# Optimization experiments

Hardware: AMD Instinct MI355X
Metric: run time of the kernel (lower is better)

## Reference

```python
import jax, jax.numpy as jnp
import numpy as np

H = 1024
R = 16


def setup_inputs() -> dict:
    key = jax.random.key(0)
    ks = jax.random.split(key, 9)
    s = 1.0 / np.sqrt(H)
    x = jax.random.normal(ks[0], (8192, H), dtype=jnp.float32)
    # gate (rule_attention): Linear(H, R)
    Wa = jax.random.uniform(ks[1], (H, R), minval=-s, maxval=s, dtype=jnp.float32)
    ba = jax.random.uniform(ks[2], (R,), minval=-s, maxval=s, dtype=jnp.float32)
    # stacked rule_heads: R x (Linear(H,H) -> ReLU -> Linear(H,H))
    W1 = jax.random.uniform(ks[3], (R, H, H), minval=-s, maxval=s, dtype=jnp.float32)
    b1 = jax.random.uniform(ks[4], (R, H), minval=-s, maxval=s, dtype=jnp.float32)
    W2 = jax.random.uniform(ks[5], (R, H, H), minval=-s, maxval=s, dtype=jnp.float32)
    b2 = jax.random.uniform(ks[6], (R, H), minval=-s, maxval=s, dtype=jnp.float32)
    # stacked rule_confidence: R x (Linear(H,1) -> Sigmoid)
    Wc = jax.random.uniform(ks[7], (R, H), minval=-s, maxval=s, dtype=jnp.float32)
    bc = jax.random.uniform(ks[8], (R,), minval=-s, maxval=s, dtype=jnp.float32)
    return {"x": x, "Wa": Wa, "ba": ba, "W1": W1, "b1": b1,
            "W2": W2, "b2": b2, "Wc": Wc, "bc": bc}


def reference(x, Wa, ba, W1, b1, W2, b2, Wc, bc):
    # gate: softmax over rules               [B, R]
    attention = jax.nn.softmax(x @ Wa + ba, axis=-1)
    # all rule MLPs as one batched matmul    [B, R, H]
    h = jax.nn.relu(jnp.einsum("bh,rhd->brd", x, W1) + b1)
    outputs = jnp.einsum("brd,rdo->bro", h, W2) + b2
    # per-rule confidence                    [B, R]
    confidences = jax.nn.sigmoid(jnp.einsum("bh,rh->br", x, Wc) + bc)
    # combine gate with confidence, renormalize, weighted sum over rules
    combined = attention * confidences
    combined = combined / (combined.sum(axis=-1, keepdims=True) + 1e-8)
    output = jnp.einsum("bro,br->bo", outputs, combined)  # [B, H]
    return output, confidences
```

## Files before the change

kernel.cpp:

```cpp
#include <hip/hip_runtime.h>

typedef __attribute__((ext_vector_type(8))) short short8;
typedef __attribute__((ext_vector_type(4))) float f32x4;

#define B_SZ 8192
#define H_SZ 1024
#define R_SZ 16

__device__ __forceinline__ unsigned short f2bf(float f) {
  union { float f; unsigned u; } v; v.f = f;
  unsigned u = v.u + 0x7FFFu + ((v.u >> 16) & 1u);
  return (unsigned short)(u >> 16);
}

__global__ __launch_bounds__(256) void cvt_bf16(const float* __restrict__ s,
                                                unsigned short* __restrict__ d) {
  size_t i = ((size_t)blockIdx.x * 256 + threadIdx.x) * 8;
  float4 f0 = *(const float4*)(s + i);
  float4 f1 = *(const float4*)(s + i + 4);
  short8 v;
  v[0] = (short)f2bf(f0.x); v[1] = (short)f2bf(f0.y);
  v[2] = (short)f2bf(f0.z); v[3] = (short)f2bf(f0.w);
  v[4] = (short)f2bf(f1.x); v[5] = (short)f2bf(f1.y);
  v[6] = (short)f2bf(f1.z); v[7] = (short)f2bf(f1.w);
  *(short8*)(d + i) = v;
}

__global__ __launch_bounds__(256) void transpose_cvt(const float* __restrict__ src,
                                                     unsigned short* __restrict__ dst,
                                                     int rows, int cols) {
  __shared__ float t[32][33];
  size_t zoff = (size_t)blockIdx.z * (size_t)rows * cols;
  int c0 = blockIdx.x * 32, r0 = blockIdx.y * 32;
  int tx = threadIdx.x, ty = threadIdx.y;
#pragma unroll
  for (int i = 0; i < 4; ++i)
    t[ty + 8 * i][tx] = src[zoff + (size_t)(r0 + ty + 8 * i) * cols + c0 + tx];
  __syncthreads();
#pragma unroll
  for (int i = 0; i < 4; ++i)
    dst[zoff + (size_t)(c0 + ty + 8 * i) * rows + r0 + tx] = f2bf(t[tx][ty + 8 * i]);
}

__global__ __launch_bounds__(64) void gate_kernel(const float* __restrict__ x,
                                                  const float* __restrict__ Wa,
                                                  const float* __restrict__ ba,
                                                  const float* __restrict__ Wc,
                                                  const float* __restrict__ bc,
                                                  float* __restrict__ comb,
                                                  float* __restrict__ conf) {
  int b = blockIdx.x, l = threadIdx.x;
  const float* xr = x + (size_t)b * H_SZ;
  float xv[16];
#pragma unroll
  for (int j = 0; j < 16; ++j) xv[j] = xr[l + 64 * j];
  float la[16], lcf[16];
#pragma unroll
  for (int r = 0; r < 16; ++r) {
    float sa = 0.f, sc = 0.f;
#pragma unroll
    for (int j = 0; j < 16; ++j) {
      int h = l + 64 * j;
      sa += xv[j] * Wa[h * 16 + r];
      sc += xv[j] * Wc[r * H_SZ + h];
    }
#pragma unroll
    for (int off = 32; off > 0; off >>= 1) {
      sa += __shfl_xor(sa, off);
      sc += __shfl_xor(sc, off);
    }
    la[r] = sa + ba[r];
    lcf[r] = sc + bc[r];
  }
  float mx = la[0];
#pragma unroll
  for (int r = 1; r < 16; ++r) mx = fmaxf(mx, la[r]);
  float se = 0.f;
#pragma unroll
  for (int r = 0; r < 16; ++r) { la[r] = expf(la[r] - mx); se += la[r]; }
  float cb[16]; float cs = 0.f;
#pragma unroll
  for (int r = 0; r < 16; ++r) {
    float cf = 1.f / (1.f + expf(-lcf[r]));
    lcf[r] = cf;
    cb[r] = (la[r] / se) * cf;
    cs += cb[r];
  }
  float inv = 1.f / (cs + 1e-8f);
  if (l < 16) {
    float cv = 0.f, qv = 0.f;
#pragma unroll
    for (int r = 0; r < 16; ++r)
      if (r == l) { cv = lcf[r]; qv = cb[r] * inv; }
    conf[b * 16 + l] = cv;
    comb[b * 16 + l] = qv;
  }
}

template <int MODE>
__global__ __launch_bounds__(256) void gemm_nt(
    const unsigned short* __restrict__ A, int lda,
    const unsigned short* __restrict__ B, int ldb, int K,
    unsigned short* __restrict__ Hp, int ldh,
    const float* __restrict__ b1v,
    float* __restrict__ Out,
    const float* __restrict__ b2v,
    const float* __restrict__ comb,
    int r_base, int accum) {
  __shared__ short smem[16384];
  short* As = smem;
  short* Bs = smem + 8192;

  const int tid = threadIdx.x;
  const int lane = tid & 63;
  const int wid = tid >> 6;
  const int wm = wid >> 1, wn = wid & 1;
  const int lr = lane >> 4, lc = lane & 15;

  const int bn0 = blockIdx.x * 128;
  const int bm0 = blockIdx.y * 128;

  int srow[4], ssc[4];
#pragma unroll
  for (int i = 0; i < 4; ++i) {
    int idx = i * 256 + tid;
    srow[i] = idx >> 3;
    ssc[i] = idx & 7;
  }

  const f32x4 zero = {0.f, 0.f, 0.f, 0.f};
  f32x4 acc[4][4];
#pragma unroll
  for (int i = 0; i < 4; ++i)
#pragma unroll
    for (int j = 0; j < 4; ++j) acc[i][j] = zero;

  const int KT = K >> 6;

  short8 va[4], vb[4];
#pragma unroll
  for (int i = 0; i < 4; ++i) {
    va[i] = *(const short8*)(A + (size_t)(bm0 + srow[i]) * lda + ssc[i] * 8);
    vb[i] = *(const short8*)(B + (size_t)(bn0 + srow[i]) * ldb + ssc[i] * 8);
  }

  for (int kt = 0; kt < KT; ++kt) {
    __syncthreads();
#pragma unroll
    for (int i = 0; i < 4; ++i) {
      *(short8*)(As + srow[i] * 64 + ((ssc[i] ^ (srow[i] & 7)) * 8)) = va[i];
      *(short8*)(Bs + srow[i] * 64 + ((ssc[i] ^ (srow[i] & 7)) * 8)) = vb[i];
    }
    __syncthreads();
    if (kt + 1 < KT) {
      int k0 = (kt + 1) << 6;
#pragma unroll
      for (int i = 0; i < 4; ++i) {
        va[i] = *(const short8*)(A + (size_t)(bm0 + srow[i]) * lda + k0 + ssc[i] * 8);
        vb[i] = *(const short8*)(B + (size_t)(bn0 + srow[i]) * ldb + k0 + ssc[i] * 8);
      }
    }
#pragma unroll
    for (int c = 0; c < 2; ++c) {
      short8 af[4], bfr[4];
#pragma unroll
      for (int f = 0; f < 4; ++f) {
        int ra = wm * 64 + f * 16 + lc;
        af[f] = *(const short8*)(As + ra * 64 + (((c * 4 + lr) ^ (ra & 7)) * 8));
        int rb = wn * 64 + f * 16 + lc;
        bfr[f] = *(const short8*)(Bs + rb * 64 + (((c * 4 + lr) ^ (rb & 7)) * 8));
      }
#pragma unroll
      for (int mf = 0; mf < 4; ++mf)
#pragma unroll
        for (int nf = 0; nf < 4; ++nf)
          acc[mf][nf] = __builtin_amdgcn_mfma_f32_16x16x32_bf16(af[mf], bfr[nf],
                                                                acc[mf][nf], 0, 0, 0);
    }
  }

#pragma unroll
  for (int mf = 0; mf < 4; ++mf) {
#pragma unroll
    for (int nf = 0; nf < 4; ++nf) {
      int m0 = bm0 + wm * 64 + mf * 16 + lr * 4;
      int n = bn0 + wn * 64 + nf * 16 + lc;
      f32x4 a = acc[mf][nf];
      if (MODE == 0) {
        int r = r_base + (n >> 10);
        int d = n & 1023;
        float bias = b1v[r * H_SZ + d];
#pragma unroll
        for (int j = 0; j < 4; ++j) {
          float v = fmaxf(a[j] + bias, 0.f) * comb[(size_t)(m0 + j) * 16 + r];
          Hp[(size_t)(m0 + j) * ldh + n] = f2bf(v);
        }
      } else {
#pragma unroll
        for (int j = 0; j < 4; ++j) {
          size_t row = (size_t)(m0 + j);
          float v = a[j];
          if (accum) {
            v += Out[row * H_SZ + n];
          } else {
            float bs = 0.f;
#pragma unroll
            for (int r = 0; r < 16; ++r)
              bs += comb[row * 16 + r] * b2v[r * H_SZ + n];
            v += bs;
          }
          Out[row * H_SZ + n] = v;
        }
      }
    }
  }
}

extern "C" void kernel_launch(void* const* d_in, const int* in_sizes, int n_in,
                              void* d_out, int out_size, void* d_ws, size_t ws_size,
                              hipStream_t stream) {
  if (n_in < 9) return;
  const float* x  = (const float*)d_in[0];
  const float* Wa = (const float*)d_in[1];
  const float* ba = (const float*)d_in[2];
  const float* W1 = (const float*)d_in[3];
  const float* b1 = (const float*)d_in[4];
  const float* W2 = (const float*)d_in[5];
  const float* b2 = (const float*)d_in[6];
  const float* Wc = (const float*)d_in[7];
  const float* bc = (const float*)d_in[8];

  float* out = (float*)d_out;
  float* conf = out + (size_t)B_SZ * H_SZ;

  char* w = (char*)d_ws;
  unsigned short* xb = (unsigned short*)w;  w += (size_t)B_SZ * H_SZ * 2;
  unsigned short* W1T = (unsigned short*)w; w += (size_t)R_SZ * H_SZ * H_SZ * 2;
  unsigned short* W2T = (unsigned short*)w; w += (size_t)R_SZ * H_SZ * H_SZ * 2;
  float* comb = (float*)w;                  w += (size_t)B_SZ * R_SZ * 4;
  unsigned short* Hp = (unsigned short*)w;
  size_t used = (size_t)(w - (char*)d_ws);

  int G = 16;
  while (G > 1 && used + (size_t)B_SZ * G * H_SZ * 2 > ws_size) G >>= 1;
  if (used + (size_t)B_SZ * G * H_SZ * 2 > ws_size) return;

  cvt_bf16<<<dim3((B_SZ * H_SZ) / (256 * 8)), dim3(256), 0, stream>>>(x, xb);
  dim3 tb(32, 8);
  transpose_cvt<<<dim3(32, 32, 16), tb, 0, stream>>>(W1, W1T, H_SZ, H_SZ);
  transpose_cvt<<<dim3(32, 512, 1), tb, 0, stream>>>(W2, W2T, R_SZ * H_SZ, H_SZ);
  gate_kernel<<<dim3(B_SZ), dim3(64), 0, stream>>>(x, Wa, ba, Wc, bc, comb, conf);

  int ngroups = R_SZ / G;
  for (int g = 0; g < ngroups; ++g) {
    gemm_nt<0><<<dim3(G * 8, 64), dim3(256), 0, stream>>>(
        xb, H_SZ,
        W1T + (size_t)g * G * H_SZ * H_SZ, H_SZ, H_SZ,
        Hp, G * H_SZ, b1, nullptr, nullptr, comb, g * G, 0);
    gemm_nt<1><<<dim3(8, 64), dim3(256), 0, stream>>>(
        Hp, G * H_SZ,
        W2T + (size_t)g * G * H_SZ, R_SZ * H_SZ, G * H_SZ,
        nullptr, 0, nullptr, out, b2, comb, 0, (g > 0) ? 1 : 0);
  }
}
```

Baseline: 780.1 us.

## Double-buffer GEMM tiles via direct global-to-LDS loads and coalesce gate weights

The GEMM main loop now loads each tile straight into LDS with global_load_lds into two alternating buffers. The next K-tile's loads are issued before the MFMAs on the current tile run, replacing the register-staged prefetch and its two barriers per step. LDS use doubles to 64KB per block, which may lower occupancy. The gate kernel now reads a transposed copy of Wa so the loads coalesce, and it packs four rows per 256-thread block.

```diff
diff --git a/kernel.cpp b/kernel.cpp
--- a/kernel.cpp
+++ b/kernel.cpp
@@ -42,14 +42,22 @@
     dst[zoff + (size_t)(c0 + ty + 8 * i) * rows + r0 + tx] = f2bf(t[tx][ty + 8 * i]);
 }
 
-__global__ __launch_bounds__(64) void gate_kernel(const float* __restrict__ x,
-                                                  const float* __restrict__ Wa,
-                                                  const float* __restrict__ ba,
-                                                  const float* __restrict__ Wc,
-                                                  const float* __restrict__ bc,
-                                                  float* __restrict__ comb,
-                                                  float* __restrict__ conf) {
-  int b = blockIdx.x, l = threadIdx.x;
+__global__ __launch_bounds__(256) void transpose_wa(const float* __restrict__ Wa,
+                                                    float* __restrict__ WaT) {
+  int t = blockIdx.x * 256 + threadIdx.x;
+  int h = t >> 4, r = t & 15;
+  WaT[r * H_SZ + h] = Wa[t];
+}
+
+__global__ __launch_bounds__(256) void gate_kernel(const float* __restrict__ x,
+                                                   const float* __restrict__ WaT,
+                                                   const float* __restrict__ ba,
+                                                   const float* __restrict__ Wc,
+                                                   const float* __restrict__ bc,
+                                                   float* __restrict__ comb,
+                                                   float* __restrict__ conf) {
+  int b = blockIdx.x * 4 + (threadIdx.x >> 6);
+  int l = threadIdx.x & 63;
   const float* xr = x + (size_t)b * H_SZ;
   float xv[16];
 #pragma unroll
@@ -61,7 +69,7 @@
 #pragma unroll
     for (int j = 0; j < 16; ++j) {
       int h = l + 64 * j;
-      sa += xv[j] * Wa[h * 16 + r];
+      sa += xv[j] * WaT[r * H_SZ + h];
       sc += xv[j] * Wc[r * H_SZ + h];
     }
 #pragma unroll
@@ -95,6 +103,12 @@
     conf[b * 16 + l] = cv;
     comb[b * 16 + l] = qv;
   }
+}
+
+__device__ __forceinline__ void gload16(const unsigned short* g, unsigned short* l) {
+  __builtin_amdgcn_global_load_lds(
+      (const __attribute__((address_space(1))) unsigned int*)g,
+      (__attribute__((address_space(3))) unsigned int*)l, 16, 0, 0);
 }
 
 template <int MODE>
@@ -107,9 +121,7 @@
     const float* __restrict__ b2v,
     const float* __restrict__ comb,
     int r_base, int accum) {
-  __shared__ short smem[16384];
-  short* As = smem;
-  short* Bs = smem + 8192;
+  __shared__ short smem[32768];
 
   const int tid = threadIdx.x;
   const int lane = tid & 63;
@@ -120,12 +132,13 @@
   const int bn0 = blockIdx.x * 128;
   const int bm0 = blockIdx.y * 128;
 
-  int srow[4], ssc[4];
+  int srow[4], schk[4], ubase[4];
 #pragma unroll
   for (int i = 0; i < 4; ++i) {
     int idx = i * 256 + tid;
     srow[i] = idx >> 3;
-    ssc[i] = idx & 7;
+    schk[i] = (idx & 7) ^ (srow[i] & 7);
+    ubase[i] = (i * 256 + (tid & 192)) * 8;
   }
 
   const f32x4 zero = {0.f, 0.f, 0.f, 0.f};
@@ -137,29 +150,26 @@
 
   const int KT = K >> 6;
 
-  short8 va[4], vb[4];
-#pragma unroll
-  for (int i = 0; i < 4; ++i) {
-    va[i] = *(const short8*)(A + (size_t)(bm0 + srow[i]) * lda + ssc[i] * 8);
-    vb[i] = *(const short8*)(B + (size_t)(bn0 + srow[i]) * ldb + ssc[i] * 8);
-  }
+  auto stage = [&](int bf, int kt) {
+    const int k0 = kt << 6;
+    short* lb = smem + bf * 16384;
+#pragma unroll
+    for (int i = 0; i < 4; ++i) {
+      gload16((const unsigned short*)A + (size_t)(bm0 + srow[i]) * lda + k0 + schk[i] * 8,
+              (unsigned short*)(lb + ubase[i]));
+      gload16((const unsigned short*)B + (size_t)(bn0 + srow[i]) * ldb + k0 + schk[i] * 8,
+              (unsigned short*)(lb + 8192 + ubase[i]));
+    }
+  };
+
+  stage(0, 0);
+  __syncthreads();
 
   for (int kt = 0; kt < KT; ++kt) {
-    __syncthreads();
-#pragma unroll
-    for (int i = 0; i < 4; ++i) {
-      *(short8*)(As + srow[i] * 64 + ((ssc[i] ^ (srow[i] & 7)) * 8)) = va[i];
-      *(short8*)(Bs + srow[i] * 64 + ((ssc[i] ^ (srow[i] & 7)) * 8)) = vb[i];
-    }
-    __syncthreads();
-    if (kt + 1 < KT) {
-      int k0 = (kt + 1) << 6;
-#pragma unroll
-      for (int i = 0; i < 4; ++i) {
-        va[i] = *(const short8*)(A + (size_t)(bm0 + srow[i]) * lda + k0 + ssc[i] * 8);
-        vb[i] = *(const short8*)(B + (size_t)(bn0 + srow[i]) * ldb + k0 + ssc[i] * 8);
-      }
-    }
+    const int cur = kt & 1;
+    if (kt + 1 < KT) stage(cur ^ 1, kt + 1);
+    const short* As = smem + cur * 16384;
+    const short* Bs = As + 8192;
 #pragma unroll
     for (int c = 0; c < 2; ++c) {
       short8 af[4], bfr[4];
@@ -177,6 +187,7 @@
           acc[mf][nf] = __builtin_amdgcn_mfma_f32_16x16x32_bf16(af[mf], bfr[nf],
                                                                 acc[mf][nf], 0, 0, 0);
     }
+    __syncthreads();
   }
 
 #pragma unroll
@@ -238,6 +249,7 @@
   unsigned short* W1T = (unsigned short*)w; w += (size_t)R_SZ * H_SZ * H_SZ * 2;
   unsigned short* W2T = (unsigned short*)w; w += (size_t)R_SZ * H_SZ * H_SZ * 2;
   float* comb = (float*)w;                  w += (size_t)B_SZ * R_SZ * 4;
+  float* WaT = (float*)w;                   w += (size_t)R_SZ * H_SZ * 4;
   unsigned short* Hp = (unsigned short*)w;
   size_t used = (size_t)(w - (char*)d_ws);
 
@@ -249,7 +261,8 @@
   dim3 tb(32, 8);
   transpose_cvt<<<dim3(32, 32, 16), tb, 0, stream>>>(W1, W1T, H_SZ, H_SZ);
   transpose_cvt<<<dim3(32, 512, 1), tb, 0, stream>>>(W2, W2T, R_SZ * H_SZ, H_SZ);
-  gate_kernel<<<dim3(B_SZ), dim3(64), 0, stream>>>(x, Wa, ba, Wc, bc, comb, conf);
+  transpose_wa<<<dim3(64), dim3(256), 0, stream>>>(Wa, WaT);
+  gate_kernel<<<dim3(B_SZ / 4), dim3(256), 0, stream>>>(x, WaT, ba, Wc, bc, comb, conf);
 
   int ngroups = R_SZ / G;
   for (int g = 0; g < ngroups; ++g) {
```

Result: faster. 761.5 us (-2.4%).
